# Optimization experiments

Hardware: AMD Instinct MI355X
Metric: run time of the kernel (lower is better)

The kernel has to match this reference:

```python
import jax, jax.numpy as jnp
import numpy as np

N_NODES = 100000
N_REL = 2
N_EDGES = 1600000  # per relation, avg degree 16
F_IN = 128
F_OUT = 64


def setup_inputs() -> dict:
    key = jax.random.key(0)
    k1, k2, k3, k4, k5 = jax.random.split(key, 5)
    x = jax.random.normal(k1, (N_NODES, F_IN), dtype=jnp.float32)
    src = jax.random.randint(k2, (N_REL, N_EDGES), 0, N_NODES)
    dst = jax.random.randint(k3, (N_REL, N_EDGES), 0, N_NODES)
    edge_w = jax.random.uniform(k4, (N_REL, N_EDGES), dtype=jnp.float32)
    # xavier_uniform with gain=1.414 as in the torch module
    limit = 1.414 * np.sqrt(6.0 / (F_IN + F_OUT))
    W = jax.random.uniform(k5, (F_IN, F_OUT), dtype=jnp.float32,
                           minval=-limit, maxval=limit)
    return {"x": x, "W": W, "edge_w": edge_w, "src": src, "dst": dst}


def reference(x, W, edge_w, src, dst):
    # Original: for each relation r, h = X @ W; support_r = A_r @ h; out = relu(sum_r support_r)
    # Since h is identical across relations and results are summed, compute
    # X @ W once and aggregate all relations' edges in one fused scatter-add.
    n = x.shape[0]
    h = x @ W  # [N, F_OUT]
    s = src.reshape(-1)  # [R*E]
    d = dst.reshape(-1)  # [R*E]
    w = edge_w.reshape(-1, 1)  # [R*E, 1]
    msgs = w * h[s]  # [R*E, F_OUT] weighted gather of source features
    agg = jax.ops.segment_sum(msgs, d, num_segments=n)  # [N, F_OUT]
    return jax.nn.relu(agg)
```

## Files before the change

kernel.cpp:

```cpp
#include <hip/hip_runtime.h>
#include <hip/hip_bf16.h>
#include <stdint.h>

#define F_IN 128
#define F_OUT 64
#define NPB 128
#define CHUNK 8192
#define NBUCK_MAX 1024
#define SRC_BITS 17
#define BCAP 5120

static __device__ __forceinline__ unsigned short f2bf(float f) {
    uint32_t u = __float_as_uint(f);
    u += 0x7FFF + ((u >> 16) & 1);
    return (unsigned short)(u >> 16);
}
static __device__ __forceinline__ float bf2f(unsigned short s) {
    return __uint_as_float((uint32_t)s << 16);
}

__global__ __launch_bounds__(256) void gemm_xw(const float* __restrict__ x,
                                               const float* __restrict__ W,
                                               unsigned short* __restrict__ h, int n,
                                               int* __restrict__ cursor) {
    __shared__ float Ws[F_IN * F_OUT];
    __shared__ float Xs[16][F_IN + 4];
    if (blockIdx.x == 0) {
        for (int i = threadIdx.x; i < NBUCK_MAX; i += 256) cursor[i] = 0;
    }
    for (int i = threadIdx.x; i < F_IN * F_OUT / 4; i += 256)
        ((float4*)Ws)[i] = ((const float4*)W)[i];
    const int row0 = blockIdx.x * 16;
    for (int i = threadIdx.x; i < 16 * 32; i += 256) {
        int r = i >> 5, c = i & 31;
        if (row0 + r < n)
            *(float4*)&Xs[r][c * 4] = *(const float4*)(x + (size_t)(row0 + r) * F_IN + c * 4);
    }
    __syncthreads();
    const int cg = threadIdx.x & 15;
    const int r  = threadIdx.x >> 4;
    const int row = row0 + r;
    float4 acc = make_float4(0.f, 0.f, 0.f, 0.f);
#pragma unroll
    for (int k4 = 0; k4 < F_IN / 4; ++k4) {
        const float4 xv = *(const float4*)&Xs[r][k4 * 4];
#pragma unroll
        for (int kk = 0; kk < 4; ++kk) {
            const float  xs = (&xv.x)[kk];
            const float4 wv = ((const float4*)Ws)[(k4 * 4 + kk) * 16 + cg];
            acc.x = fmaf(xs, wv.x, acc.x);
            acc.y = fmaf(xs, wv.y, acc.y);
            acc.z = fmaf(xs, wv.z, acc.z);
            acc.w = fmaf(xs, wv.w, acc.w);
        }
    }
    if (row < n) {
        ushort4 o;
        o.x = f2bf(acc.x); o.y = f2bf(acc.y); o.z = f2bf(acc.z); o.w = f2bf(acc.w);
        *(ushort4*)(h + (size_t)row * F_OUT + cg * 4) = o;
    }
}

__global__ __launch_bounds__(512) void partA(const int* __restrict__ src,
                                             const int* __restrict__ dst,
                                             const float* __restrict__ ew,
                                             int* __restrict__ cursor,
                                             uint32_t* __restrict__ rec32,
                                             uint8_t* __restrict__ dlo8,
                                             long nE, int nbuck) {
    __shared__ uint32_t srec[CHUNK];
    __shared__ uint8_t  sdlo[CHUNK];
    __shared__ int cnt[NBUCK_MAX];
    __shared__ int lbase[NBUCK_MAX];
    __shared__ int gbase[NBUCK_MAX];
    int* const ssc = gbase;
    const int c   = blockIdx.x;
    const int tid = threadIdx.x;
    const long base = (long)c * CHUNK;
    const long endl = base + CHUNK < nE ? base + CHUNK : nE;
    const int tcount = (int)(endl - base);

    for (int i = tid; i < NBUCK_MAX; i += 512) cnt[i] = 0;
    __syncthreads();
    for (int i = tid; i < tcount; i += 512)
        atomicAdd(&cnt[dst[base + i] >> 7], 1);
    __syncthreads();
    {
        const int t2 = tid * 2;
        const int a0 = cnt[t2], a1 = cnt[t2 + 1];
        const int ts = a0 + a1;
        ssc[tid] = ts; __syncthreads();
        for (int o = 1; o < 512; o <<= 1) {
            int t = (tid >= o) ? ssc[tid - o] : 0;
            __syncthreads();
            ssc[tid] += t;
            __syncthreads();
        }
        const int excl = ssc[tid] - ts;
        lbase[t2] = excl;
        lbase[t2 + 1] = excl + a0;
    }
    __syncthreads();
    for (int k = tid; k < nbuck; k += 512) {
        const int ck = cnt[k];
        if (ck) gbase[k] = k * BCAP + atomicAdd(&cursor[k], ck);
    }
    __syncthreads();
    for (int i = tid; i < NBUCK_MAX; i += 512) cnt[i] = lbase[i];
    __syncthreads();
    for (int i = tid; i < tcount; i += 512) {
        const int d = dst[base + i];
        const int k = d >> 7;
        const int pos = atomicAdd(&cnt[k], 1);
        uint32_t u = __float_as_uint(ew[base + i]);
        u += 0x10000u;
        srec[pos] = (u & 0xFFFE0000u) | (uint32_t)src[base + i];
        sdlo[pos] = (uint8_t)(d & (NPB - 1));
    }
    __syncthreads();
    for (int j = tid; j < tcount; j += 512) {
        int k = 0;
#pragma unroll
        for (int s = 512; s > 0; s >>= 1) {
            const int nk = k + s;
            if (nk < NBUCK_MAX && lbase[nk] <= j) k = nk;
        }
        const int gpos = gbase[k] + (j - lbase[k]);
        rec32[gpos] = srec[j];
        dlo8[gpos]  = sdlo[j];
    }
}

__global__ __launch_bounds__(256) void sortB(uint32_t* __restrict__ rec,
                                             const uint8_t* __restrict__ dlo8,
                                             const int* __restrict__ cursor,
                                             int* __restrict__ obeg,
                                             int* __restrict__ oend,
                                             int n, int nbuck) {
    __shared__ uint32_t ssort[BCAP];
    __shared__ int cnt[NPB], run[NPB], sa[NPB], sb[NPB];
    const int k   = blockIdx.x;
    const int tid = threadIdx.x;
    const int rbase = k * BCAP;
    int m = cursor[k];
    if (m > BCAP) m = BCAP;
    if (tid < NPB) cnt[tid] = 0;
    __syncthreads();
    for (int i = tid; i < m; i += 256)
        atomicAdd(&cnt[dlo8[(long)rbase + i]], 1);
    __syncthreads();
    if (tid < NPB) sa[tid] = cnt[tid];
    __syncthreads();
    int* pin = sa; int* pout = sb;
    for (int o = 1; o < NPB; o <<= 1) {
        if (tid < NPB) pout[tid] = pin[tid] + (tid >= o ? pin[tid - o] : 0);
        __syncthreads();
        int* t = pin; pin = pout; pout = t;
    }
    if (tid < NPB) {
        const int e = pin[tid] - cnt[tid];
        run[tid] = e;
        const int node = k * NPB + tid;
        if (node < n) {
            obeg[node] = rbase + e;
            oend[node] = rbase + e + cnt[tid];
        }
    }
    __syncthreads();
    for (int i = tid; i < m; i += 256) {
        const uint32_t r = rec[(long)rbase + i];
        const int d = dlo8[(long)rbase + i];
        ssort[atomicAdd(&run[d], 1)] = r;
    }
    __syncthreads();
    for (int i = tid; i < m; i += 256)
        rec[(long)rbase + i] = ssort[i];
}

__global__ __launch_bounds__(256, 8) void gather_nodes(
        const unsigned short* __restrict__ h,
        const uint32_t* __restrict__ rec,
        const int* __restrict__ obeg,
        const int* __restrict__ oend,
        float* __restrict__ out, int n) {
    const int wid   = threadIdx.x >> 6;
    const int lane  = threadIdx.x & 63;
    const int lhalf = lane >> 5;
    const int lidx  = lane & 31;
    const int node = blockIdx.x * 4 + wid;
    if (node >= n) return;
    int j = obeg[node];
    const int end = oend[node];
    const uint32_t M = (1u << SRC_BITS) - 1;
    const uint32_t* __restrict__ h2 = (const uint32_t*)h;
    float accx = 0.f, accy = 0.f;

    auto pair = [&](uint32_t r0, uint32_t r1) {
        const uint32_t rs = lhalf ? r1 : r0;
        const uint32_t d  = h2[(rs & M) * 32u + lidx];
        const float w = __uint_as_float(rs & 0xFFFE0000u);
        accx = fmaf(w, __uint_as_float(d << 16), accx);
        accy = fmaf(w, __uint_as_float(d & 0xFFFF0000u), accy);
    };

    for (; j < end && (j & 3); ++j) {
        const uint32_t r = rec[j];
        pair(r, r & M);
    }
    for (; j + 8 <= end; j += 8) {
        const uint4 A = *(const uint4*)(rec + j);
        const uint4 B = *(const uint4*)(rec + j + 4);
        pair(A.x, A.y);
        pair(A.z, A.w);
        pair(B.x, B.y);
        pair(B.z, B.w);
    }
    if (j + 4 <= end) {
        const uint4 A = *(const uint4*)(rec + j);
        pair(A.x, A.y);
        pair(A.z, A.w);
        j += 4;
    }
    if (j + 2 <= end) {
        const uint2 A = *(const uint2*)(rec + j);
        pair(A.x, A.y);
        j += 2;
    }
    if (j < end) {
        const uint32_t r = rec[j];
        pair(r, r & M);
    }
    accx += __shfl_xor(accx, 32);
    accy += __shfl_xor(accy, 32);
    if (lane < 32) {
        float2 o;
        o.x = fmaxf(accx, 0.f);
        o.y = fmaxf(accy, 0.f);
        ((float2*)(out + (size_t)node * F_OUT))[lidx] = o;
    }
}

__global__ __launch_bounds__(256) void scatter_edges(const unsigned short* __restrict__ h,
                                                     const float* __restrict__ edge_w,
                                                     const int* __restrict__ src,
                                                     const int* __restrict__ dst,
                                                     float* __restrict__ out, long n_edges) {
    const int lane = threadIdx.x & 63;
    const long wave = ((long)blockIdx.x * blockDim.x + threadIdx.x) >> 6;
    const long nwaves = ((long)gridDim.x * blockDim.x) >> 6;
    for (long e = wave; e < n_edges; e += nwaves) {
        const float v = edge_w[e] * bf2f(h[(size_t)src[e] * F_OUT + lane]);
        atomicAdd(&out[(size_t)dst[e] * F_OUT + lane], v);
    }
}

__global__ __launch_bounds__(256) void relu_inplace(float* __restrict__ out, long n4) {
    long i = (long)blockIdx.x * blockDim.x + threadIdx.x;
    const long stride = (long)gridDim.x * blockDim.x;
    float4* p = (float4*)out;
    for (; i < n4; i += stride) {
        float4 v = p[i];
        v.x = v.x > 0.f ? v.x : 0.f;
        v.y = v.y > 0.f ? v.y : 0.f;
        v.z = v.z > 0.f ? v.z : 0.f;
        v.w = v.w > 0.f ? v.w : 0.f;
        p[i] = v;
    }
}

extern "C" void kernel_launch(void* const* d_in, const int* in_sizes, int n_in,
                              void* d_out, int out_size, void* d_ws, size_t ws_size,
                              hipStream_t stream) {
    const float* x      = (const float*)d_in[0];
    const float* W      = (const float*)d_in[1];
    const float* edge_w = (const float*)d_in[2];
    const int*   src    = (const int*)d_in[3];
    const int*   dst    = (const int*)d_in[4];
    float*       out    = (float*)d_out;

    const int  n_nodes = in_sizes[0] / F_IN;
    const long nE      = (long)in_sizes[2];
    const int  NBUCK   = (n_nodes + NPB - 1) / NPB;
    const int  NCHUNK  = (int)((nE + CHUNK - 1) / CHUNK);
    const int  gemmB   = (n_nodes + 15) / 16;

    size_t off = 0;
    auto seg = [&](size_t bytes) { size_t p = off; off = (off + bytes + 255) & ~(size_t)255; return p; };
    const size_t h_off    = seg((size_t)n_nodes * F_OUT * sizeof(unsigned short));
    const size_t rec_off  = seg((size_t)NBUCK * BCAP * sizeof(uint32_t));
    const size_t dlo_off  = seg((size_t)NBUCK * BCAP * sizeof(uint8_t));
    const size_t cur_off  = seg(NBUCK_MAX * sizeof(int));
    const size_t obeg_off = seg((size_t)n_nodes * sizeof(int));
    const size_t oend_off = seg((size_t)n_nodes * sizeof(int));
    char* ws = (char*)d_ws;

    unsigned short* h = (unsigned short*)(ws + h_off);

    if (off <= ws_size && NBUCK <= NBUCK_MAX && n_nodes <= (1 << SRC_BITS)) {
        uint32_t* rec    = (uint32_t*)(ws + rec_off);
        uint8_t*  dlo8   = (uint8_t*)(ws + dlo_off);
        int*      cursor = (int*)(ws + cur_off);
        int*      obeg   = (int*)(ws + obeg_off);
        int*      oend   = (int*)(ws + oend_off);

        gemm_xw<<<gemmB, 256, 0, stream>>>(x, W, h, n_nodes, cursor);
        partA<<<NCHUNK, 512, 0, stream>>>(src, dst, edge_w, cursor, rec, dlo8, nE, NBUCK);
        sortB<<<NBUCK, 256, 0, stream>>>(rec, dlo8, cursor, obeg, oend, n_nodes, NBUCK);
        gather_nodes<<<(n_nodes + 3) / 4, 256, 0, stream>>>(h, rec, obeg, oend, out, n_nodes);
    } else {
        int* cursor = (int*)d_ws;
        gemm_xw<<<gemmB, 256, 0, stream>>>(x, W, h, n_nodes, cursor);
        hipMemsetAsync(d_out, 0, (size_t)out_size * sizeof(float), stream);
        scatter_edges<<<2048, 256, 0, stream>>>(h, edge_w, src, dst, out, nE);
        relu_inplace<<<1024, 256, 0, stream>>>(out, (long)out_size / 4);
    }
}
```

Measured before the change: 171.4 us.

## Fuse GEMM and edge partitioning into one heterogeneous launch

```diff
diff --git a/kernel.cpp b/kernel.cpp
--- a/kernel.cpp
+++ b/kernel.cpp
@@ -9,6 +9,7 @@
 #define NBUCK_MAX 1024
 #define SRC_BITS 17
 #define BCAP 5120
+#define GROWS 32
 
 static __device__ __forceinline__ unsigned short f2bf(float f) {
     uint32_t u = __float_as_uint(f);
@@ -19,26 +20,94 @@
     return __uint_as_float((uint32_t)s << 16);
 }
 
-__global__ __launch_bounds__(256) void gemm_xw(const float* __restrict__ x,
-                                               const float* __restrict__ W,
-                                               unsigned short* __restrict__ h, int n,
-                                               int* __restrict__ cursor) {
-    __shared__ float Ws[F_IN * F_OUT];
-    __shared__ float Xs[16][F_IN + 4];
-    if (blockIdx.x == 0) {
-        for (int i = threadIdx.x; i < NBUCK_MAX; i += 256) cursor[i] = 0;
-    }
-    for (int i = threadIdx.x; i < F_IN * F_OUT / 4; i += 256)
+__global__ __launch_bounds__(512) void fusedA(
+        const float* __restrict__ x, const float* __restrict__ W,
+        unsigned short* __restrict__ h, int n,
+        const int* __restrict__ src, const int* __restrict__ dst,
+        const float* __restrict__ ew, int* __restrict__ cursor,
+        uint32_t* __restrict__ rec32, uint8_t* __restrict__ dlo8,
+        long nE, int nbuck, int partBlocks) {
+    __shared__ __align__(16) char smem[53248];
+    const int tid = threadIdx.x;
+
+    if ((int)blockIdx.x < partBlocks) {
+        uint32_t* srec  = (uint32_t*)smem;
+        uint8_t*  sdlo  = (uint8_t*)(smem + 32768);
+        int*      cnt   = (int*)(smem + 40960);
+        int*      lbase = (int*)(smem + 45056);
+        int*      gbase = (int*)(smem + 49152);
+        int* const ssc  = gbase;
+        const int  c      = blockIdx.x;
+        const long base   = (long)c * CHUNK;
+        const long endl   = base + CHUNK < nE ? base + CHUNK : nE;
+        const int  tcount = (int)(endl - base);
+
+        for (int i = tid; i < NBUCK_MAX; i += 512) cnt[i] = 0;
+        __syncthreads();
+        for (int i = tid; i < tcount; i += 512)
+            atomicAdd(&cnt[dst[base + i] >> 7], 1);
+        __syncthreads();
+        {
+            const int t2 = tid * 2;
+            const int a0 = cnt[t2], a1 = cnt[t2 + 1];
+            const int ts = a0 + a1;
+            ssc[tid] = ts; __syncthreads();
+            for (int o = 1; o < 512; o <<= 1) {
+                int t = (tid >= o) ? ssc[tid - o] : 0;
+                __syncthreads();
+                ssc[tid] += t;
+                __syncthreads();
+            }
+            const int excl = ssc[tid] - ts;
+            lbase[t2] = excl;
+            lbase[t2 + 1] = excl + a0;
+        }
+        __syncthreads();
+        for (int k = tid; k < nbuck; k += 512) {
+            const int ck = cnt[k];
+            if (ck) gbase[k] = k * BCAP + atomicAdd(&cursor[k], ck);
+        }
+        __syncthreads();
+        for (int i = tid; i < NBUCK_MAX; i += 512) cnt[i] = lbase[i];
+        __syncthreads();
+        for (int i = tid; i < tcount; i += 512) {
+            const int d = dst[base + i];
+            const int k = d >> 7;
+            const int pos = atomicAdd(&cnt[k], 1);
+            uint32_t u = __float_as_uint(ew[base + i]);
+            u += 0x10000u;
+            srec[pos] = (u & 0xFFFE0000u) | (uint32_t)src[base + i];
+            sdlo[pos] = (uint8_t)(d & (NPB - 1));
+        }
+        __syncthreads();
+        for (int j = tid; j < tcount; j += 512) {
+            int k = 0;
+#pragma unroll
+            for (int s = 512; s > 0; s >>= 1) {
+                const int nk = k + s;
+                if (nk < NBUCK_MAX && lbase[nk] <= j) k = nk;
+            }
+            const int gpos = gbase[k] + (j - lbase[k]);
+            rec32[gpos] = srec[j];
+            dlo8[gpos]  = sdlo[j];
+        }
+        return;
+    }
+
+    float* Ws = (float*)smem;
+    float (*Xs)[F_IN + 4] = (float(*)[F_IN + 4])(smem + F_IN * F_OUT * 4);
+    const int gb = (int)blockIdx.x - partBlocks;
+    for (int i = tid; i < F_IN * F_OUT / 4; i += 512)
         ((float4*)Ws)[i] = ((const float4*)W)[i];
-    const int row0 = blockIdx.x * 16;
-    for (int i = threadIdx.x; i < 16 * 32; i += 256) {
+    const int row0 = gb * GROWS;
+    for (int i = tid; i < GROWS * 32; i += 512) {
         int r = i >> 5, c = i & 31;
         if (row0 + r < n)
             *(float4*)&Xs[r][c * 4] = *(const float4*)(x + (size_t)(row0 + r) * F_IN + c * 4);
     }
     __syncthreads();
-    const int cg = threadIdx.x & 15;
-    const int r  = threadIdx.x >> 4;
+    const int cg = tid & 15;
+    const int r  = tid >> 4;
     const int row = row0 + r;
     float4 acc = make_float4(0.f, 0.f, 0.f, 0.f);
 #pragma unroll
@@ -58,76 +127,6 @@
         ushort4 o;
         o.x = f2bf(acc.x); o.y = f2bf(acc.y); o.z = f2bf(acc.z); o.w = f2bf(acc.w);
         *(ushort4*)(h + (size_t)row * F_OUT + cg * 4) = o;
-    }
-}
-
-__global__ __launch_bounds__(512) void partA(const int* __restrict__ src,
-                                             const int* __restrict__ dst,
-                                             const float* __restrict__ ew,
-                                             int* __restrict__ cursor,
-                                             uint32_t* __restrict__ rec32,
-                                             uint8_t* __restrict__ dlo8,
-                                             long nE, int nbuck) {
-    __shared__ uint32_t srec[CHUNK];
-    __shared__ uint8_t  sdlo[CHUNK];
-    __shared__ int cnt[NBUCK_MAX];
-    __shared__ int lbase[NBUCK_MAX];
-    __shared__ int gbase[NBUCK_MAX];
-    int* const ssc = gbase;
-    const int c   = blockIdx.x;
-    const int tid = threadIdx.x;
-    const long base = (long)c * CHUNK;
-    const long endl = base + CHUNK < nE ? base + CHUNK : nE;
-    const int tcount = (int)(endl - base);
-
-    for (int i = tid; i < NBUCK_MAX; i += 512) cnt[i] = 0;
-    __syncthreads();
-    for (int i = tid; i < tcount; i += 512)
-        atomicAdd(&cnt[dst[base + i] >> 7], 1);
-    __syncthreads();
-    {
-        const int t2 = tid * 2;
-        const int a0 = cnt[t2], a1 = cnt[t2 + 1];
-        const int ts = a0 + a1;
-        ssc[tid] = ts; __syncthreads();
-        for (int o = 1; o < 512; o <<= 1) {
-            int t = (tid >= o) ? ssc[tid - o] : 0;
-            __syncthreads();
-            ssc[tid] += t;
-            __syncthreads();
-        }
-        const int excl = ssc[tid] - ts;
-        lbase[t2] = excl;
-        lbase[t2 + 1] = excl + a0;
-    }
-    __syncthreads();
-    for (int k = tid; k < nbuck; k += 512) {
-        const int ck = cnt[k];
-        if (ck) gbase[k] = k * BCAP + atomicAdd(&cursor[k], ck);
-    }
-    __syncthreads();
-    for (int i = tid; i < NBUCK_MAX; i += 512) cnt[i] = lbase[i];
-    __syncthreads();
-    for (int i = tid; i < tcount; i += 512) {
-        const int d = dst[base + i];
-        const int k = d >> 7;
-        const int pos = atomicAdd(&cnt[k], 1);
-        uint32_t u = __float_as_uint(ew[base + i]);
-        u += 0x10000u;
-        srec[pos] = (u & 0xFFFE0000u) | (uint32_t)src[base + i];
-        sdlo[pos] = (uint8_t)(d & (NPB - 1));
-    }
-    __syncthreads();
-    for (int j = tid; j < tcount; j += 512) {
-        int k = 0;
-#pragma unroll
-        for (int s = 512; s > 0; s >>= 1) {
-            const int nk = k + s;
-            if (nk < NBUCK_MAX && lbase[nk] <= j) k = nk;
-        }
-        const int gpos = gbase[k] + (j - lbase[k]);
-        rec32[gpos] = srec[j];
-        dlo8[gpos]  = sdlo[j];
     }
 }
 
@@ -240,6 +239,40 @@
     }
 }
 
+__global__ __launch_bounds__(256) void gemm_only(const float* __restrict__ x,
+                                                 const float* __restrict__ W,
+                                                 unsigned short* __restrict__ h, int n) {
+    __shared__ float Ws[F_IN * F_OUT];
+    __shared__ float Xs[16][F_IN + 4];
+    for (int i = threadIdx.x; i < F_IN * F_OUT / 4; i += 256)
+        ((float4*)Ws)[i] = ((const float4*)W)[i];
+    const int row0 = blockIdx.x * 16;
+    for (int i = threadIdx.x; i < 16 * 32; i += 256) {
+        int r = i >> 5, c = i & 31;
+        if (row0 + r < n)
+            *(float4*)&Xs[r][c * 4] = *(const float4*)(x + (size_t)(row0 + r) * F_IN + c * 4);
+    }
+    __syncthreads();
+    const int cg = threadIdx.x & 15;
+    const int r  = threadIdx.x >> 4;
+    const int row = row0 + r;
+    float4 acc = make_float4(0.f, 0.f, 0.f, 0.f);
+#pragma unroll
+    for (int k = 0; k < F_IN; ++k) {
+        float  xv = Xs[r][k];
+        float4 wv = ((const float4*)Ws)[k * 16 + cg];
+        acc.x = fmaf(xv, wv.x, acc.x);
+        acc.y = fmaf(xv, wv.y, acc.y);
+        acc.z = fmaf(xv, wv.z, acc.z);
+        acc.w = fmaf(xv, wv.w, acc.w);
+    }
+    if (row < n) {
+        ushort4 o;
+        o.x = f2bf(acc.x); o.y = f2bf(acc.y); o.z = f2bf(acc.z); o.w = f2bf(acc.w);
+        *(ushort4*)(h + (size_t)row * F_OUT + cg * 4) = o;
+    }
+}
+
 __global__ __launch_bounds__(256) void scatter_edges(const unsigned short* __restrict__ h,
                                                      const float* __restrict__ edge_w,
                                                      const int* __restrict__ src,
@@ -282,7 +315,7 @@
     const long nE      = (long)in_sizes[2];
     const int  NBUCK   = (n_nodes + NPB - 1) / NPB;
     const int  NCHUNK  = (int)((nE + CHUNK - 1) / CHUNK);
-    const int  gemmB   = (n_nodes + 15) / 16;
+    const int  gemmB   = (n_nodes + GROWS - 1) / GROWS;
 
     size_t off = 0;
     auto seg = [&](size_t bytes) { size_t p = off; off = (off + bytes + 255) & ~(size_t)255; return p; };
@@ -303,13 +336,14 @@
         int*      obeg   = (int*)(ws + obeg_off);
         int*      oend   = (int*)(ws + oend_off);
 
-        gemm_xw<<<gemmB, 256, 0, stream>>>(x, W, h, n_nodes, cursor);
-        partA<<<NCHUNK, 512, 0, stream>>>(src, dst, edge_w, cursor, rec, dlo8, nE, NBUCK);
+        hipMemsetAsync(cursor, 0, NBUCK_MAX * sizeof(int), stream);
+        fusedA<<<NCHUNK + gemmB, 512, 0, stream>>>(x, W, h, n_nodes,
+                                                   src, dst, edge_w, cursor,
+                                                   rec, dlo8, nE, NBUCK, NCHUNK);
         sortB<<<NBUCK, 256, 0, stream>>>(rec, dlo8, cursor, obeg, oend, n_nodes, NBUCK);
         gather_nodes<<<(n_nodes + 3) / 4, 256, 0, stream>>>(h, rec, obeg, oend, out, n_nodes);
     } else {
-        int* cursor = (int*)d_ws;
-        gemm_xw<<<gemmB, 256, 0, stream>>>(x, W, h, n_nodes, cursor);
+        gemm_only<<<(n_nodes + 15) / 16, 256, 0, stream>>>(x, W, h, n_nodes);
         hipMemsetAsync(d_out, 0, (size_t)out_size * sizeof(float), stream);
         scatter_edges<<<2048, 256, 0, stream>>>(h, edge_w, src, dst, out, nE);
         relu_inplace<<<1024, 256, 0, stream>>>(out, (long)out_size / 4);
```

After: 157.0 us. 8.4% less time.
